# Performance work log

Hardware: AMD Instinct MI355X
Metric: run time of the kernel (lower is better)

The kernel has to match this reference:

```python
import jax, jax.numpy as jnp
import numpy as np

N_HEAD = 12
N_EMBD = 768


def setup_inputs() -> dict:
    key = jax.random.key(0)
    k1, k2, k3, k4, k5 = jax.random.split(key, 5)
    B, T, C = 4, 2048, N_EMBD
    s = 0.02
    x = jax.random.normal(k1, (B, T, C), dtype=jnp.float32)
    w_attn = jax.random.normal(k2, (C, 3 * C), dtype=jnp.float32) * s
    b_attn = jnp.zeros((3 * C,), dtype=jnp.float32)
    w_proj = jax.random.normal(k3, (C, C), dtype=jnp.float32) * s
    b_proj = jnp.zeros((C,), dtype=jnp.float32)
    return {"x": x, "w_attn": w_attn, "b_attn": b_attn, "w_proj": w_proj, "b_proj": b_proj}


def reference(x, w_attn, b_attn, w_proj, b_proj):
    # dropout omitted (eval mode / dropout=0.0)
    B, T, C = x.shape
    H = N_HEAD
    D = C // H  # head dim
    qkv = x @ w_attn + b_attn                      # [B,T,3C]
    q, k, v = jnp.split(qkv, 3, axis=-1)
    q = q.reshape(B, T, H, D).transpose(0, 2, 1, 3)  # [B,H,T,D]
    k = k.reshape(B, T, H, D).transpose(0, 2, 1, 3)
    v = v.reshape(B, T, H, D).transpose(0, 2, 1, 3)
    att = jnp.einsum('bhqd,bhkd->bhqk', q, k) * (1.0 / np.sqrt(D))  # [B,H,T,T]
    causal = jnp.tril(jnp.ones((T, T), dtype=bool))
    att = jnp.where(causal[None, None], att, -jnp.inf)
    att = jax.nn.softmax(att, axis=-1)
    y = jnp.einsum('bhqk,bhkd->bhqd', att, v)      # [B,H,T,D]
    y = y.transpose(0, 2, 1, 3).reshape(B, T, C)
    return y @ w_proj + b_proj
```

## Files before the change

### kernel.cpp

```cpp
#include <hip/hip_runtime.h>
#include <stdint.h>

typedef unsigned short ushort_t;

#define T_SEQ 2048
#define BATCH 4
#define NHEAD 12
#define CEMB 768
#define HDIM 64
#define C3 2304

__device__ __forceinline__ ushort_t f2b_hw(float f) {
  union { __bf16 h; ushort_t u; } p;
  p.h = (__bf16)f;
  return p.u;
}
__device__ __forceinline__ uint32_t pkbf16(float lo, float hi) {
  union { __bf16 h[2]; uint32_t u; } p;
  p.h[0] = (__bf16)lo; p.h[1] = (__bf16)hi;
  return p.u;
}

typedef __attribute__((address_space(3))) unsigned int lds_u32_t;
typedef const __attribute__((address_space(1))) unsigned int glb_u32_t;
__device__ __forceinline__ void async_cp16(const void* g, void* l) {
  __builtin_amdgcn_global_load_lds((glb_u32_t*)g, (lds_u32_t*)l, 16, 0, 0);
}

__global__ __launch_bounds__(256) void prep_k(const float* __restrict__ x, ushort_t* __restrict__ xb,
                                              const float* __restrict__ wa, ushort_t* __restrict__ wT,
                                              const float* __restrict__ wp, ushort_t* __restrict__ wpT) {
  const int blk = blockIdx.x;
  const int tid = threadIdx.x;
  if (blk < 3072) {
    const int i = blk * 256 + tid;
    float4 a = ((const float4*)x)[2 * i];
    float4 b = ((const float4*)x)[2 * i + 1];
    uint4 v;
    v.x = pkbf16(a.x, a.y); v.y = pkbf16(a.z, a.w);
    v.z = pkbf16(b.x, b.y); v.w = pkbf16(b.z, b.w);
    ((uint4*)xb)[i] = v;
    return;
  }
  __shared__ ushort_t tile[32][33];
  const float* in; ushort_t* out; int R, C, bx, by;
  if (blk < 4800) {
    const int t = blk - 3072;
    in = wa; out = wT; R = CEMB; C = C3;
    bx = t % 72; by = t / 72;
  } else {
    const int t = blk - 4800;
    in = wp; out = wpT; R = CEMB; C = CEMB;
    bx = t % 24; by = t / 24;
  }
  const int tx = tid & 31, ty = tid >> 5;
  const int c0 = bx * 32, r0 = by * 32;
  for (int i = ty; i < 32; i += 8)
    tile[i][tx] = f2b_hw(in[(size_t)(r0 + i) * C + c0 + tx]);
  __syncthreads();
  for (int i = ty; i < 32; i += 8)
    out[(size_t)(c0 + i) * R + r0 + tx] = tile[tx][i];
}

typedef __bf16 bf16x8 __attribute__((ext_vector_type(8)));
typedef float f32x4 __attribute__((ext_vector_type(4)));
typedef short short4_t __attribute__((ext_vector_type(4)));

template <bool OUTF, int BM>
__global__ __launch_bounds__(256) void gemm_bt(const ushort_t* __restrict__ A,
                                               const ushort_t* __restrict__ Bt,
                                               const float* __restrict__ bias,
                                               void* __restrict__ Cv,
                                               int M, int N, int K) {
  constexpr int TM = BM / 32;
  __shared__ ushort_t As[2 * BM * 32];
  __shared__ ushort_t Bs[2 * 128 * 32];
  const int tid = threadIdx.x;
  const int m0 = blockIdx.y * BM, n0 = blockIdx.x * 128;
  const int wid = tid >> 6, lane = tid & 63;
  const int quad = lane >> 4, l15 = lane & 15;
  const int wm = (wid >> 1) * (BM / 2), wn = (wid & 1) * 64;
  f32x4 acc[TM][4] = {};

  const int e0 = tid * 8;
  const int r0s = e0 >> 5, c0s = e0 & 31;
  const int e1 = e0 + 2048;
  const int r1s = e1 >> 5, c1s = e1 & 31;

  for (int k0 = 0; k0 < K; k0 += 64) {
    __syncthreads();
#pragma unroll
    for (int p = 0; p < 2; p++) {
      const int kc = k0 + p * 32;
      async_cp16(&A[(size_t)(m0 + r0s) * K + kc + c0s], &As[p * BM * 32 + e0]);
      if constexpr (BM == 128)
        async_cp16(&A[(size_t)(m0 + r1s) * K + kc + c1s], &As[p * BM * 32 + e1]);
      async_cp16(&Bt[(size_t)(n0 + r0s) * K + kc + c0s], &Bs[p * 128 * 32 + e0]);
      async_cp16(&Bt[(size_t)(n0 + r1s) * K + kc + c1s], &Bs[p * 128 * 32 + e1]);
    }
    __syncthreads();
    bf16x8 af[TM][2], bfr[4][2];
#pragma unroll
    for (int t = 0; t < TM; t++)
#pragma unroll
      for (int p = 0; p < 2; p++)
        af[t][p] = *(const bf16x8*)&As[p * BM * 32 + (wm + t * 16 + l15) * 32 + quad * 8];
#pragma unroll
    for (int t = 0; t < 4; t++)
#pragma unroll
      for (int p = 0; p < 2; p++)
        bfr[t][p] = *(const bf16x8*)&Bs[p * 128 * 32 + (wn + t * 16 + l15) * 32 + quad * 8];
#pragma unroll
    for (int p = 0; p < 2; p++)
#pragma unroll
      for (int tm = 0; tm < TM; tm++)
#pragma unroll
        for (int tn = 0; tn < 4; tn++)
          acc[tm][tn] = __builtin_amdgcn_mfma_f32_16x16x32_bf16(af[tm][p], bfr[tn][p], acc[tm][tn], 0, 0, 0);
  }

#pragma unroll
  for (int tm = 0; tm < TM; tm++) {
    const int row = m0 + wm + tm * 16 + quad * 4;
#pragma unroll
    for (int tn = 0; tn < 4; tn++) {
      const int col = n0 + wn + tn * 16 + l15;
      const float bv = bias[col];
#pragma unroll
      for (int rr = 0; rr < 4; rr++) {
        if constexpr (OUTF)
          ((float*)Cv)[(size_t)(row + rr) * N + col] = acc[tm][tn][rr] + bv;
        else
          ((ushort_t*)Cv)[(size_t)(row + rr) * N + col] = f2b_hw(acc[tm][tn][rr] + bv);
      }
    }
  }
}

#define VSTR 64

__device__ __forceinline__ void commit_v(ushort_t* __restrict__ vt, const int* __restrict__ offs,
                                         uint4 pV0, uint4 pV1) {
  union { uint32_t u[4]; uint4 v; } a, c;
  a.v = pV0; c.v = pV1;
#pragma unroll
  for (int j = 0; j < 8; j++) {
    uint32_t pk = __builtin_amdgcn_perm(c.u[j >> 1], a.u[j >> 1],
                                        (j & 1) ? 0x07060302u : 0x05040100u);
    *(uint32_t*)&vt[offs[j]] = pk;
  }
}

__global__ __launch_bounds__(256, 4) void attn_mfma_k(const ushort_t* __restrict__ qkv,
                                                      ushort_t* __restrict__ y) {
  __shared__ ushort_t Ksm[2][2][64 * 32];
  __shared__ ushort_t Vt[2][64 * VSTR];

  const int by = blockIdx.y;
  const int qt = (by & 1) ? (by >> 1) : (15 - (by >> 1));
  const int h = blockIdx.x >> 2, b = blockIdx.x & 3;
  const int tid = threadIdx.x;
  const int w = tid >> 6, lane = tid & 63;
  const int quad = lane >> 4, l15 = lane & 15;
  const int nkt = 2 * qt + 2;
  const int qw = qt * 128 + w * 32;

  const int e0 = tid * 8;
  const int kchunk = (tid & 3) ^ ((tid >> 3) & 3);
  const ushort_t* kbase = qkv + ((size_t)(b * T_SEQ) + (tid >> 2)) * C3 + CEMB + h * HDIM + kchunk * 8;
  const int vpair = tid & 31, vd0 = (tid >> 5) * 8;
  const ushort_t* vbase = qkv + ((size_t)(b * T_SEQ) + 2 * vpair) * C3 + 2 * CEMB + h * HDIM + vd0;
  const size_t step = (size_t)64 * C3;

  int voffw[8];
#pragma unroll
  for (int j = 0; j < 8; j++)
    voffw[j] = (vd0 + j) * VSTR + (((vpair >> 2) ^ j) << 3) + ((vpair & 3) << 1);

  const int sw7 = l15 & 7;
  int koff[4];
#pragma unroll
  for (int m = 0; m < 4; m++)
    koff[m] = (m * 16 + l15) * 32 + ((quad ^ ((l15 >> 1) & 3)) << 3);
  int vbrow[4], vcm[4];
#pragma unroll
  for (int nd = 0; nd < 4; nd++)
    vbrow[nd] = (nd * 16 + l15) * VSTR + ((quad & 1) << 2);
#pragma unroll
  for (int m = 0; m < 4; m++)
    vcm[m] = ((2 * m + (quad >> 1)) ^ sw7) << 3;

  const int qrel0 = w * 32 + l15;
  const int qrel1 = qrel0 + 16;

  const float C2 = 0.18033688011112042f;

  bf16x8 qB[2][2];
#pragma unroll
  for (int qf = 0; qf < 2; qf++)
#pragma unroll
    for (int kb = 0; kb < 2; kb++)
      qB[qf][kb] = *(const bf16x8*)&qkv[((size_t)(b * T_SEQ + qw + qf * 16 + l15)) * C3 +
                                        h * HDIM + kb * 32 + quad * 8];

  f32x4 o2[2][4] = {};
  float m0 = -3e38f, m1 = -3e38f;
  float lq0 = 0.f, lq1 = 0.f;

  const ushort_t* kp = kbase;
  const ushort_t* vp = vbase;
  uint4 pV0 = *(const uint4*)vp, pV1 = *(const uint4*)(vp + C3);
  async_cp16(kp, &Ksm[0][0][e0]);
  async_cp16(kp + 32, &Ksm[0][1][e0]);
  commit_v(Vt[0], voffw, pV0, pV1);
  vp += step;
  pV0 = *(const uint4*)vp; pV1 = *(const uint4*)(vp + C3);

  for (int kt = 0; kt < nkt; ++kt) {
    __syncthreads();
    if (kt + 1 < nkt) {
      const int nb = (kt + 1) & 1;
      kp += step;
      async_cp16(kp, &Ksm[nb][0][e0]);
      async_cp16(kp + 32, &Ksm[nb][1][e0]);
      commit_v(Vt[nb], voffw, pV0, pV1);
      if (kt + 2 < nkt) {
        vp += step;
        pV0 = *(const uint4*)vp; pV1 = *(const uint4*)(vp + C3);
      }
    }
    const int cb = kt & 1;

    bf16x8 kA[4][2];
#pragma unroll
    for (int m = 0; m < 4; m++) {
      kA[m][0] = *(const bf16x8*)&Ksm[cb][0][koff[m]];
      kA[m][1] = *(const bf16x8*)&Ksm[cb][1][koff[m]];
    }
    f32x4 st0[4] = {}, st1[4] = {};
#pragma unroll
    for (int m = 0; m < 4; m++) {
      st0[m] = __builtin_amdgcn_mfma_f32_16x16x32_bf16(kA[m][0], qB[0][0], st0[m], 0, 0, 0);
      st0[m] = __builtin_amdgcn_mfma_f32_16x16x32_bf16(kA[m][1], qB[0][1], st0[m], 0, 0, 0);
      st1[m] = __builtin_amdgcn_mfma_f32_16x16x32_bf16(kA[m][0], qB[1][0], st1[m], 0, 0, 0);
      st1[m] = __builtin_amdgcn_mfma_f32_16x16x32_bf16(kA[m][1], qB[1][1], st1[m], 0, 0, 0);
    }

    if (kt >= nkt - 2) {
      const int krel = (kt << 6) - (qt << 7) + quad * 4;
#pragma unroll
      for (int m = 0; m < 4; m++)
#pragma unroll
        for (int r = 0; r < 4; r++) {
          const int kr = krel + m * 16 + r;
          if (kr > qrel0) st0[m][r] = -3e38f;
          if (kr > qrel1) st1[m][r] = -3e38f;
        }
    }

    f32x4 mq0, mq1;
#pragma unroll
    for (int r = 0; r < 4; r++) {
      mq0[r] = fmaxf(fmaxf(st0[0][r], st0[1][r]), fmaxf(st0[2][r], st0[3][r]));
      mq1[r] = fmaxf(fmaxf(st1[0][r], st1[1][r]), fmaxf(st1[2][r], st1[3][r]));
    }
    const float mx0 = fmaxf(fmaxf(mq0[0], mq0[1]), fmaxf(mq0[2], mq0[3]));
    const float mx1 = fmaxf(fmaxf(mq1[0], mq1[1]), fmaxf(mq1[2], mq1[3]));

    float al0 = 1.f, al1 = 1.f;
    const bool viol = (mx0 - m0 > 22.18f) || (mx1 - m1 > 22.18f);
    if (__any(viol)) {
      float a = fmaxf(mx0, __shfl_xor(mx0, 16, 64));
      a = fmaxf(a, __shfl_xor(a, 32, 64));
      float bm = fmaxf(mx1, __shfl_xor(mx1, 16, 64));
      bm = fmaxf(bm, __shfl_xor(bm, 32, 64));
      const float n0 = fmaxf(m0, a), n1 = fmaxf(m1, bm);
      al0 = exp2f((m0 - n0) * C2);
      al1 = exp2f((m1 - n1) * C2);
      m0 = n0; m1 = n1;
#pragma unroll
      for (int nd = 0; nd < 4; nd++)
#pragma unroll
        for (int r = 0; r < 4; r++) {
          o2[0][nd][r] *= al0;
          o2[1][nd][r] *= al1;
        }
    }
    const float mnc0 = m0 * C2, mnc1 = m1 * C2;
#pragma unroll
    for (int m = 0; m < 4; m++)
#pragma unroll
      for (int r = 0; r < 4; r++) {
        st0[m][r] = exp2f(fmaf(st0[m][r], C2, -mnc0));
        st1[m][r] = exp2f(fmaf(st1[m][r], C2, -mnc1));
      }
    f32x4 s40, s41;
#pragma unroll
    for (int r = 0; r < 4; r++) {
      s40[r] = (st0[0][r] + st0[1][r]) + (st0[2][r] + st0[3][r]);
      s41[r] = (st1[0][r] + st1[1][r]) + (st1[2][r] + st1[3][r]);
    }
    lq0 = fmaf(lq0, al0, (s40[0] + s40[1]) + (s40[2] + s40[3]));
    lq1 = fmaf(lq1, al1, (s41[0] + s41[1]) + (s41[2] + s41[3]));

    short4_t pf0[4], pf1[4];
#pragma unroll
    for (int m = 0; m < 4; m++) {
      union { uint32_t u[2]; short4_t s; } pa, pb;
      pa.u[0] = pkbf16(st0[m][0], st0[m][1]);
      pa.u[1] = pkbf16(st0[m][2], st0[m][3]);
      pb.u[0] = pkbf16(st1[m][0], st1[m][1]);
      pb.u[1] = pkbf16(st1[m][2], st1[m][3]);
      pf0[m] = pa.s; pf1[m] = pb.s;
    }

#pragma unroll
    for (int m = 0; m < 4; m++)
#pragma unroll
      for (int nd = 0; nd < 4; nd++) {
        const short4_t vv = *(const short4_t*)&Vt[cb][vbrow[nd] + vcm[m]];
        o2[0][nd] = __builtin_amdgcn_mfma_f32_16x16x16bf16_1k(vv, pf0[m], o2[0][nd], 0, 0, 0);
        o2[1][nd] = __builtin_amdgcn_mfma_f32_16x16x16bf16_1k(vv, pf1[m], o2[1][nd], 0, 0, 0);
      }
  }

  {
    float lt0 = lq0 + __shfl_xor(lq0, 16, 64);
    lt0 += __shfl_xor(lt0, 32, 64);
    float lt1 = lq1 + __shfl_xor(lq1, 16, 64);
    lt1 += __shfl_xor(lt1, 32, 64);
    const float inv0 = 1.0f / lt0, inv1 = 1.0f / lt1;
#pragma unroll
    for (int qf = 0; qf < 2; qf++) {
      const float inv = qf ? inv1 : inv0;
      const int qg = qw + qf * 16 + l15;
      ushort_t* yp = y + ((size_t)(b * T_SEQ + qg)) * CEMB + h * HDIM + quad * 4;
#pragma unroll
      for (int nd = 0; nd < 4; nd++) {
        uint2 pk;
        pk.x = pkbf16(o2[qf][nd][0] * inv, o2[qf][nd][1] * inv);
        pk.y = pkbf16(o2[qf][nd][2] * inv, o2[qf][nd][3] * inv);
        *(uint2*)(yp + nd * 16) = pk;
      }
    }
  }
}

extern "C" void kernel_launch(void* const* d_in, const int* in_sizes, int n_in,
                              void* d_out, int out_size, void* d_ws, size_t ws_size,
                              hipStream_t stream) {
  const float* x      = (const float*)d_in[0];
  const float* w_attn = (const float*)d_in[1];
  const float* b_attn = (const float*)d_in[2];
  const float* w_proj = (const float*)d_in[3];
  const float* b_proj = (const float*)d_in[4];
  float* out = (float*)d_out;

  char* ws = (char*)d_ws;
  ushort_t* qkv = (ushort_t*)ws;
  ushort_t* y   = qkv + (size_t)8192 * 2304;
  ushort_t* xb  = y + (size_t)8192 * 768;
  ushort_t* wT  = xb + (size_t)8192 * 768;
  ushort_t* wpT = wT + (size_t)2304 * 768;

  prep_k<<<5376, 256, 0, stream>>>(x, xb, w_attn, wT, w_proj, wpT);

  gemm_bt<false, 128><<<dim3(C3 / 128, 8192 / 128), 256, 0, stream>>>(xb, wT, b_attn, qkv, 8192, C3, CEMB);

  attn_mfma_k<<<dim3(48, 16), 256, 0, stream>>>(qkv, y);

  gemm_bt<true, 64><<<dim3(CEMB / 128, 8192 / 64), 256, 0, stream>>>(y, wpT, b_proj, out, 8192, CEMB, CEMB);
}
```

Measured before the change: 239.6 us.

## Switch PV to 16x16x32 MFMA, double-buffer GEMM stages, simplify attention scheduling

The attention PV product now uses the 16x16x32 bf16 MFMA with 8-wide fragments. To make the score layout match, K rows are loaded in a permuted order and the causal mask indices are remapped. The GEMM loop moves from loading 64-wide K chunks with two barriers to a software-pipelined double buffer of 32-wide stages, prefetching the next stage while the current one computes. The attention kernel also drops the interleaved q-tile ordering for a plain descending order and lowers the launch-bounds occupancy hint from 4 to 3. Together these aim to halve PV MFMA instruction count and hide GEMM load latency, at the cost of register pressure and possible load imbalance.

```diff
diff --git a/kernel.cpp b/kernel.cpp
--- a/kernel.cpp
+++ b/kernel.cpp
@@ -64,7 +64,6 @@
 
 typedef __bf16 bf16x8 __attribute__((ext_vector_type(8)));
 typedef float f32x4 __attribute__((ext_vector_type(4)));
-typedef short short4_t __attribute__((ext_vector_type(4)));
 
 template <bool OUTF, int BM>
 __global__ __launch_bounds__(256) void gemm_bt(const ushort_t* __restrict__ A,
@@ -73,8 +72,8 @@
                                                void* __restrict__ Cv,
                                                int M, int N, int K) {
   constexpr int TM = BM / 32;
-  __shared__ ushort_t As[2 * BM * 32];
-  __shared__ ushort_t Bs[2 * 128 * 32];
+  __shared__ ushort_t As[2][BM * 32];
+  __shared__ ushort_t Bs[2][128 * 32];
   const int tid = threadIdx.x;
   const int m0 = blockIdx.y * BM, n0 = blockIdx.x * 128;
   const int wid = tid >> 6, lane = tid & 63;
@@ -87,37 +86,37 @@
   const int e1 = e0 + 2048;
   const int r1s = e1 >> 5, c1s = e1 & 31;
 
-  for (int k0 = 0; k0 < K; k0 += 64) {
+  const int KS = K >> 5;
+
+#define GSTAGE(ks, bf)                                                              \
+  {                                                                                 \
+    const int kc = (ks) << 5;                                                       \
+    async_cp16(&A[(size_t)(m0 + r0s) * K + kc + c0s], &As[bf][e0]);                 \
+    if constexpr (BM == 128)                                                        \
+      async_cp16(&A[(size_t)(m0 + r1s) * K + kc + c1s], &As[bf][e1]);               \
+    async_cp16(&Bt[(size_t)(n0 + r0s) * K + kc + c0s], &Bs[bf][e0]);                \
+    async_cp16(&Bt[(size_t)(n0 + r1s) * K + kc + c1s], &Bs[bf][e1]);                \
+  }
+
+  GSTAGE(0, 0);
+  for (int ks = 0; ks < KS; ks++) {
+    const int pb = ks & 1;
     __syncthreads();
-#pragma unroll
-    for (int p = 0; p < 2; p++) {
-      const int kc = k0 + p * 32;
-      async_cp16(&A[(size_t)(m0 + r0s) * K + kc + c0s], &As[p * BM * 32 + e0]);
-      if constexpr (BM == 128)
-        async_cp16(&A[(size_t)(m0 + r1s) * K + kc + c1s], &As[p * BM * 32 + e1]);
-      async_cp16(&Bt[(size_t)(n0 + r0s) * K + kc + c0s], &Bs[p * 128 * 32 + e0]);
-      async_cp16(&Bt[(size_t)(n0 + r1s) * K + kc + c1s], &Bs[p * 128 * 32 + e1]);
-    }
-    __syncthreads();
-    bf16x8 af[TM][2], bfr[4][2];
+    if (ks + 1 < KS) GSTAGE(ks + 1, pb ^ 1);
+    bf16x8 af[TM], bfr[4];
 #pragma unroll
     for (int t = 0; t < TM; t++)
-#pragma unroll
-      for (int p = 0; p < 2; p++)
-        af[t][p] = *(const bf16x8*)&As[p * BM * 32 + (wm + t * 16 + l15) * 32 + quad * 8];
+      af[t] = *(const bf16x8*)&As[pb][(wm + t * 16 + l15) * 32 + quad * 8];
 #pragma unroll
     for (int t = 0; t < 4; t++)
-#pragma unroll
-      for (int p = 0; p < 2; p++)
-        bfr[t][p] = *(const bf16x8*)&Bs[p * 128 * 32 + (wn + t * 16 + l15) * 32 + quad * 8];
-#pragma unroll
-    for (int p = 0; p < 2; p++)
-#pragma unroll
-      for (int tm = 0; tm < TM; tm++)
-#pragma unroll
-        for (int tn = 0; tn < 4; tn++)
-          acc[tm][tn] = __builtin_amdgcn_mfma_f32_16x16x32_bf16(af[tm][p], bfr[tn][p], acc[tm][tn], 0, 0, 0);
-  }
+      bfr[t] = *(const bf16x8*)&Bs[pb][(wn + t * 16 + l15) * 32 + quad * 8];
+#pragma unroll
+    for (int tm = 0; tm < TM; tm++)
+#pragma unroll
+      for (int tn = 0; tn < 4; tn++)
+        acc[tm][tn] = __builtin_amdgcn_mfma_f32_16x16x32_bf16(af[tm], bfr[tn], acc[tm][tn], 0, 0, 0);
+  }
+#undef GSTAGE
 
 #pragma unroll
   for (int tm = 0; tm < TM; tm++) {
@@ -151,13 +150,12 @@
   }
 }
 
-__global__ __launch_bounds__(256, 4) void attn_mfma_k(const ushort_t* __restrict__ qkv,
+__global__ __launch_bounds__(256, 3) void attn_mfma_k(const ushort_t* __restrict__ qkv,
                                                       ushort_t* __restrict__ y) {
   __shared__ ushort_t Ksm[2][2][64 * 32];
   __shared__ ushort_t Vt[2][64 * VSTR];
 
-  const int by = blockIdx.y;
-  const int qt = (by & 1) ? (by >> 1) : (15 - (by >> 1));
+  const int qt = 15 - blockIdx.y;
   const int h = blockIdx.x >> 2, b = blockIdx.x & 3;
   const int tid = threadIdx.x;
   const int w = tid >> 6, lane = tid & 63;
@@ -166,8 +164,11 @@
   const int qw = qt * 128 + w * 32;
 
   const int e0 = tid * 8;
-  const int kchunk = (tid & 3) ^ ((tid >> 3) & 3);
-  const ushort_t* kbase = qkv + ((size_t)(b * T_SEQ) + (tid >> 2)) * C3 + CEMB + h * HDIM + kchunk * 8;
+  const int p_slot = tid >> 2;
+  const int key_true = ((p_slot >> 5) << 5) | (((p_slot >> 2) & 3) << 3) |
+                       (((p_slot >> 4) & 1) << 2) | (p_slot & 3);
+  const int kchunk = (tid & 3) ^ ((p_slot >> 1) & 3);
+  const ushort_t* kbase = qkv + ((size_t)(b * T_SEQ) + key_true) * C3 + CEMB + h * HDIM + kchunk * 8;
   const int vpair = tid & 31, vd0 = (tid >> 5) * 8;
   const ushort_t* vbase = qkv + ((size_t)(b * T_SEQ) + 2 * vpair) * C3 + 2 * CEMB + h * HDIM + vd0;
   const size_t step = (size_t)64 * C3;
@@ -182,13 +183,12 @@
 #pragma unroll
   for (int m = 0; m < 4; m++)
     koff[m] = (m * 16 + l15) * 32 + ((quad ^ ((l15 >> 1) & 3)) << 3);
-  int vbrow[4], vcm[4];
-#pragma unroll
-  for (int nd = 0; nd < 4; nd++)
-    vbrow[nd] = (nd * 16 + l15) * VSTR + ((quad & 1) << 2);
-#pragma unroll
-  for (int m = 0; m < 4; m++)
-    vcm[m] = ((2 * m + (quad >> 1)) ^ sw7) << 3;
+  int vroff[2][4];
+#pragma unroll
+  for (int a2 = 0; a2 < 2; a2++)
+#pragma unroll
+    for (int nd = 0; nd < 4; nd++)
+      vroff[a2][nd] = (nd * 16 + l15) * VSTR + (((4 * a2 + quad) ^ sw7) << 3);
 
   const int qrel0 = w * 32 + l15;
   const int qrel1 = qrel0 + 16;
@@ -247,15 +247,17 @@
     }
 
     if (kt >= nkt - 2) {
-      const int krel = (kt << 6) - (qt << 7) + quad * 4;
-#pragma unroll
-      for (int m = 0; m < 4; m++)
+      const int kb0 = (kt << 6) - (qt << 7) + quad * 8;
+#pragma unroll
+      for (int m = 0; m < 4; m++) {
+        const int bm = kb0 + ((m >> 1) << 5) + ((m & 1) << 2);
 #pragma unroll
         for (int r = 0; r < 4; r++) {
-          const int kr = krel + m * 16 + r;
+          const int kr = bm + r;
           if (kr > qrel0) st0[m][r] = -3e38f;
           if (kr > qrel1) st1[m][r] = -3e38f;
         }
+      }
     }
 
     f32x4 mq0, mq1;
@@ -303,24 +305,28 @@
     lq0 = fmaf(lq0, al0, (s40[0] + s40[1]) + (s40[2] + s40[3]));
     lq1 = fmaf(lq1, al1, (s41[0] + s41[1]) + (s41[2] + s41[3]));
 
-    short4_t pf0[4], pf1[4];
-#pragma unroll
-    for (int m = 0; m < 4; m++) {
-      union { uint32_t u[2]; short4_t s; } pa, pb;
-      pa.u[0] = pkbf16(st0[m][0], st0[m][1]);
-      pa.u[1] = pkbf16(st0[m][2], st0[m][3]);
-      pb.u[0] = pkbf16(st1[m][0], st1[m][1]);
-      pb.u[1] = pkbf16(st1[m][2], st1[m][3]);
-      pf0[m] = pa.s; pf1[m] = pb.s;
-    }
-
-#pragma unroll
-    for (int m = 0; m < 4; m++)
+    bf16x8 pf0[2], pf1[2];
+#pragma unroll
+    for (int a2 = 0; a2 < 2; a2++) {
+      union { uint32_t u[4]; bf16x8 v; } pa, pb;
+      pa.u[0] = pkbf16(st0[2 * a2][0], st0[2 * a2][1]);
+      pa.u[1] = pkbf16(st0[2 * a2][2], st0[2 * a2][3]);
+      pa.u[2] = pkbf16(st0[2 * a2 + 1][0], st0[2 * a2 + 1][1]);
+      pa.u[3] = pkbf16(st0[2 * a2 + 1][2], st0[2 * a2 + 1][3]);
+      pb.u[0] = pkbf16(st1[2 * a2][0], st1[2 * a2][1]);
+      pb.u[1] = pkbf16(st1[2 * a2][2], st1[2 * a2][3]);
+      pb.u[2] = pkbf16(st1[2 * a2 + 1][0], st1[2 * a2 + 1][1]);
+      pb.u[3] = pkbf16(st1[2 * a2 + 1][2], st1[2 * a2 + 1][3]);
+      pf0[a2] = pa.v; pf1[a2] = pb.v;
+    }
+
+#pragma unroll
+    for (int a2 = 0; a2 < 2; a2++)
 #pragma unroll
       for (int nd = 0; nd < 4; nd++) {
-        const short4_t vv = *(const short4_t*)&Vt[cb][vbrow[nd] + vcm[m]];
-        o2[0][nd] = __builtin_amdgcn_mfma_f32_16x16x16bf16_1k(vv, pf0[m], o2[0][nd], 0, 0, 0);
-        o2[1][nd] = __builtin_amdgcn_mfma_f32_16x16x16bf16_1k(vv, pf1[m], o2[1][nd], 0, 0, 0);
+        const bf16x8 vv = *(const bf16x8*)&Vt[cb][vroff[a2][nd]];
+        o2[0][nd] = __builtin_amdgcn_mfma_f32_16x16x32_bf16(vv, pf0[a2], o2[0][nd], 0, 0, 0);
+        o2[1][nd] = __builtin_amdgcn_mfma_f32_16x16x32_bf16(vv, pf1[a2], o2[1][nd], 0, 0, 0);
       }
   }
 
```

Result: faster. 221.2 us (-7.7%).
